# Kernel optimization log

Measured on AMD Instinct MI355X. Metric: run time of the kernel, lower is better.

## Reference

```python
import jax, jax.numpy as jnp
import numpy as np

B, S, D, H, F = 4, 2048, 1024, 16, 4096
HD = D // H
NEG = -2.0 ** 32
EPS = 1e-5


def _gelu(x):
    return x * 0.5 * (1.0 + jax.scipy.special.erf(x / jnp.sqrt(2.0).astype(x.dtype)))


def _layernorm(x, scale, offset):
    mu = jnp.mean(x, axis=-1, keepdims=True)
    var = jnp.mean(jnp.square(x - mu), axis=-1, keepdims=True)
    return (x - mu) * jax.lax.rsqrt(var + EPS) * scale + offset


def setup_inputs() -> dict:
    key = jax.random.key(0)
    ks = jax.random.split(key, 12)
    s = 0.02
    return {
        "x": jax.random.normal(ks[0], (B, S, D), jnp.float32),
        "mask": jnp.zeros((B, S), jnp.int32),  # 1 = masked-out (padding)
        "Wq": jax.random.normal(ks[1], (D, D), jnp.float32) * s,
        "bq": jnp.zeros((D,), jnp.float32),
        "Wk": jax.random.normal(ks[2], (D, D), jnp.float32) * s,
        "bk": jnp.zeros((D,), jnp.float32),
        "Wv": jax.random.normal(ks[3], (D, D), jnp.float32) * s,
        "bv": jnp.zeros((D,), jnp.float32),
        "Wo": jax.random.normal(ks[4], (D, D), jnp.float32) * s,
        "bo": jnp.zeros((D,), jnp.float32),
        "ln1_s": jnp.ones((D,), jnp.float32),
        "ln1_b": jnp.zeros((D,), jnp.float32),
        "W1": jax.random.normal(ks[5], (D, F), jnp.float32) * s,
        "b1": jnp.zeros((F,), jnp.float32),
        "W2": jax.random.normal(ks[6], (F, D), jnp.float32) * s,
        "b2": jnp.zeros((D,), jnp.float32),
        "ln2_s": jnp.ones((D,), jnp.float32),
        "ln2_b": jnp.zeros((D,), jnp.float32),
    }


def reference(x, mask, Wq, bq, Wk, bk, Wv, bv, Wo, bo, ln1_s, ln1_b,
              W1, b1, W2, b2, ln2_s, ln2_b):
    b, s, d = x.shape
    q = (x @ Wq + bq).reshape(b, s, H, HD)
    k = (x @ Wk + bk).reshape(b, s, H, HD)
    v = (x @ Wv + bv).reshape(b, s, H, HD)
    logits = jnp.einsum('btnh,bsnh->bnts', q, k) / jnp.sqrt(jnp.float32(HD))
    logits = logits + (mask.astype(jnp.float32) * NEG)[:, None, None, :]
    attn = jax.nn.softmax(logits, axis=-1)
    ctx = jnp.einsum('bsnh,bnts->btnh', v, attn).reshape(b, s, d)
    attn_out = ctx @ Wo + bo
    h = _layernorm(attn_out + x, ln1_s, ln1_b)
    mlp = _gelu(h @ W1 + b1) @ W2 + b2
    return _layernorm(mlp + h, ln2_s, ln2_b)
```

## Files before the change

kernel.cpp:

```cpp
#include <hip/hip_runtime.h>
#include <hip/hip_bf16.h>

typedef __attribute__((ext_vector_type(8))) short short8;
typedef __attribute__((ext_vector_type(4))) short s16x4;
typedef __attribute__((ext_vector_type(4))) float f32x4;
typedef unsigned short u16;

#define DEV __device__ __forceinline__
#define MFMA32(a, b, c) __builtin_amdgcn_mfma_f32_16x16x32_bf16(a, b, c, 0, 0, 0)
#define MFMA16(a, b, c) __builtin_amdgcn_mfma_f32_16x16x16bf16_1k(a, b, c, 0, 0, 0)

DEV u16 f2b(float f) {
    __hip_bfloat16 h = __float2bfloat16(f);
    return __builtin_bit_cast(unsigned short, h);
}

DEV void gl_lds16(const u16* g, u16* l) {
    __builtin_amdgcn_global_load_lds((const unsigned int*)g, (unsigned int*)l, 16, 0, 0);
}

__global__ __launch_bounds__(256) void cast_bf16(const float* __restrict__ in, u16* __restrict__ out, int n) {
    int i = (blockIdx.x * 256 + threadIdx.x) * 4;
    if (i < n) {
        float4 v = *(const float4*)(in + i);
        ushort4 o;
        o.x = f2b(v.x); o.y = f2b(v.y); o.z = f2b(v.z); o.w = f2b(v.w);
        *(ushort4*)(out + i) = o;
    }
}

__global__ __launch_bounds__(256) void transpose_cast(const float* __restrict__ in, u16* __restrict__ out,
                                                      int R, int C) {
    __shared__ float t[32][33];
    int bx = blockIdx.x * 32;
    int by = blockIdx.y * 32;
    int tx = threadIdx.x, ty = threadIdx.y;
#pragma unroll
    for (int i = 0; i < 32; i += 8) t[ty + i][tx] = in[(size_t)(by + ty + i) * C + bx + tx];
    __syncthreads();
#pragma unroll
    for (int i = 0; i < 32; i += 8) out[(size_t)(bx + ty + i) * R + by + tx] = f2b(t[tx][ty + i]);
}

__global__ __launch_bounds__(256) void pack_bias(const float* __restrict__ bq, const float* __restrict__ bk,
                                                 const float* __restrict__ bv, const float* __restrict__ bo,
                                                 const float* __restrict__ b1, const float* __restrict__ b2,
                                                 float* __restrict__ out) {
    int i = blockIdx.x * 256 + threadIdx.x;
    if (i >= 9216) return;
    float v;
    if (i < 1024) v = bq[i];
    else if (i < 2048) v = bk[i - 1024];
    else if (i < 3072) v = bv[i - 2048];
    else if (i < 4096) v = bo[i - 3072];
    else if (i < 8192) v = b1[i - 4096];
    else v = b2[i - 8192];
    out[i] = v;
}

template <bool GELU, bool BF16OUT>
__global__ __launch_bounds__(256) void gemm_bt(const u16* __restrict__ A, const u16* __restrict__ B,
                                               const float* __restrict__ bias, float* __restrict__ cf,
                                               u16* __restrict__ cb, int M, int N, int K) {
    __shared__ __align__(16) u16 As[128 * 32];
    __shared__ __align__(16) u16 Bs[128 * 32];
    const int tid = threadIdx.x;
    const int wid = tid >> 6, lane = tid & 63;
    const int wr = wid >> 1, wc = wid & 1;
    const int m0 = blockIdx.x * 128, n0 = blockIdx.y * 128;
    const int r16 = lane & 15, g = lane >> 4;
    const int lrow = lane >> 2, lk = (lane & 3) * 8;

    f32x4 acc[4][4];
#pragma unroll
    for (int i = 0; i < 4; i++)
#pragma unroll
        for (int j = 0; j < 4; j++) acc[i][j] = (f32x4){0.f, 0.f, 0.f, 0.f};

    const u16* ga = A + (size_t)(m0 + wid * 32 + lrow) * K + lk;
    const u16* gb = B + (size_t)(n0 + wid * 32 + lrow) * K + lk;
    u16* lA0 = &As[(wid * 32) * 32];
    u16* lA1 = &As[(wid * 32 + 16) * 32];
    u16* lB0 = &Bs[(wid * 32) * 32];
    u16* lB1 = &Bs[(wid * 32 + 16) * 32];

    for (int kt = 0; kt < K; kt += 32) {
        gl_lds16(ga + kt, lA0);
        gl_lds16(ga + (size_t)16 * K + kt, lA1);
        gl_lds16(gb + kt, lB0);
        gl_lds16(gb + (size_t)16 * K + kt, lB1);
        __syncthreads();
        short8 af[4], bfr[4];
#pragma unroll
        for (int i = 0; i < 4; i++) af[i] = *(const short8*)&As[(wr * 64 + i * 16 + r16) * 32 + g * 8];
#pragma unroll
        for (int j = 0; j < 4; j++) bfr[j] = *(const short8*)&Bs[(wc * 64 + j * 16 + r16) * 32 + g * 8];
#pragma unroll
        for (int i = 0; i < 4; i++)
#pragma unroll
            for (int j = 0; j < 4; j++) acc[i][j] = MFMA32(af[i], bfr[j], acc[i][j]);
        __syncthreads();
    }

#pragma unroll
    for (int i = 0; i < 4; i++) {
#pragma unroll
        for (int j = 0; j < 4; j++) {
#pragma unroll
            for (int r = 0; r < 4; r++) {
                int row = m0 + wr * 64 + i * 16 + g * 4 + r;
                int col = n0 + wc * 64 + j * 16 + r16;
                float v = acc[i][j][r] + bias[col];
                if (GELU) v = 0.5f * v * (1.0f + erff(v * 0.70710678118654752f));
                if (BF16OUT) cb[(size_t)row * N + col] = f2b(v);
                else cf[(size_t)row * N + col] = v;
            }
        }
    }
}

__global__ __launch_bounds__(256) void attn_kernel(const u16* __restrict__ qkv, const int* __restrict__ mask,
                                                   u16* __restrict__ ctx) {
    const int tid = threadIdx.x, wid = tid >> 6, lane = tid & 63;
    const int r16 = lane & 15, g = lane >> 4;
    const int h = blockIdx.y, b = blockIdx.z;
    const size_t baserow = (size_t)b * 2048;
    const int q0 = blockIdx.x * 64;

    __shared__ __align__(16) u16 Ks[64 * 64];
    __shared__ __align__(16) u16 Vs[64 * 64];
    __shared__ __align__(16) float mb[64];

    const float SCALE = 0.18033688011112042f;
    const float MNEG = -6.196328018e9f;

    short8 qf0, qf1;
    {
        const u16* qp = qkv + (baserow + q0 + wid * 16 + r16) * 3072 + h * 64 + g * 8;
        qf0 = *(const short8*)qp;
        qf1 = *(const short8*)(qp + 32);
    }

    const int L = lane;
    const int kchunk = (L & 7) ^ (L >> 3);
    const u16* kg0 = qkv + (baserow + wid * 16 + (L >> 3)) * 3072 + 1024 + h * 64 + kchunk * 8;
    const u16* kg1 = kg0 + (size_t)8 * 3072;
    u16* kl0 = &Ks[wid * 1024];
    u16* kl1 = &Ks[wid * 1024 + 512];
    const u16* vg0 = qkv + (baserow + wid * 16 + ((L & 31) >> 1)) * 3072 + 2048 + h * 64
                     + ((L >> 5) * 16 + (L & 1) * 8);
    const u16* vg1 = vg0 + 32;
    u16* vl0 = &Vs[wid * 1024];
    u16* vl1 = &Vs[wid * 1024 + 512];
    const unsigned vaddr = (unsigned)(unsigned long long)&Vs[0] + (unsigned)(r16 * 2 + g * 128);

    f32x4 Ot[4];
#pragma unroll
    for (int dt = 0; dt < 4; dt++) Ot[dt] = (f32x4){0.f, 0.f, 0.f, 0.f};
    float mrun = -1e30f, lrun = 0.f;

    for (int kt = 0; kt < 2048; kt += 64) {
        const size_t go = (size_t)kt * 3072;
        gl_lds16(kg0 + go, kl0);
        gl_lds16(kg1 + go, kl1);
        gl_lds16(vg0 + go, vl0);
        gl_lds16(vg1 + go, vl1);
        if (tid < 64) mb[tid] = mask[baserow + kt + tid] ? MNEG : 0.0f;
        __syncthreads();

        f32x4 z[4];
#pragma unroll
        for (int t = 0; t < 4; t++) {
            const int row = t * 16 + r16;
            const int sw = row & 7;
            short8 a0 = *(const short8*)&Ks[row * 64 + ((g ^ sw) * 8)];
            short8 a1 = *(const short8*)&Ks[row * 64 + (((4 + g) ^ sw) * 8)];
            f32x4 zz = (f32x4){0.f, 0.f, 0.f, 0.f};
            zz = MFMA32(a0, qf0, zz);
            zz = MFMA32(a1, qf1, zz);
            z[t] = zz;
        }

        f32x4 sv[4];
#pragma unroll
        for (int t = 0; t < 4; t++) {
            f32x4 mbv = *(const f32x4*)&mb[t * 16 + g * 4];
            sv[t] = z[t] * SCALE + mbv;
        }

        float pmax = sv[0][0];
#pragma unroll
        for (int t = 0; t < 4; t++)
#pragma unroll
            for (int j = 0; j < 4; j++) pmax = fmaxf(pmax, sv[t][j]);
        pmax = fmaxf(pmax, __shfl_xor(pmax, 16));
        pmax = fmaxf(pmax, __shfl_xor(pmax, 32));

        if (!__all(pmax - mrun <= 11.5f)) {
            float mnew = fmaxf(mrun, pmax);
            float alpha = exp2f(mrun - mnew);
            mrun = mnew;
            lrun *= alpha;
#pragma unroll
            for (int dt = 0; dt < 4; dt++) Ot[dt] *= alpha;
        }

        s16x4 pb[4];
        float rs = 0.f;
#pragma unroll
        for (int t = 0; t < 4; t++) {
            float p0 = exp2f(sv[t][0] - mrun);
            float p1 = exp2f(sv[t][1] - mrun);
            float p2 = exp2f(sv[t][2] - mrun);
            float p3 = exp2f(sv[t][3] - mrun);
            rs += (p0 + p1) + (p2 + p3);
            s16x4 pk;
            pk[0] = (short)f2b(p0); pk[1] = (short)f2b(p1);
            pk[2] = (short)f2b(p2); pk[3] = (short)f2b(p3);
            pb[t] = pk;
        }
        rs += __shfl_xor(rs, 16);
        rs += __shfl_xor(rs, 32);
        lrun += rs;

        s16x4 vf[4][4];
#pragma unroll
        for (int t = 0; t < 4; t++)
#pragma unroll
            for (int dt = 0; dt < 4; dt++)
                asm volatile("ds_read_b64_tr_b16 %0, %1"
                             : "=v"(vf[t][dt])
                             : "v"(vaddr + (unsigned)((t * 4 + dt) * 512)));
        asm volatile("s_waitcnt lgkmcnt(0)" ::: "memory");
        __builtin_amdgcn_sched_barrier(0);
#pragma unroll
        for (int t = 0; t < 4; t++)
#pragma unroll
            for (int dt = 0; dt < 4; dt++) Ot[dt] = MFMA16(vf[t][dt], pb[t], Ot[dt]);
        __syncthreads();
    }

    const float rl = 1.0f / lrun;
    u16* cp = ctx + (baserow + q0 + wid * 16 + r16) * 1024 + h * 64 + g * 4;
#pragma unroll
    for (int dt = 0; dt < 4; dt++) {
        ushort4 o4;
        o4.x = f2b(Ot[dt][0] * rl);
        o4.y = f2b(Ot[dt][1] * rl);
        o4.z = f2b(Ot[dt][2] * rl);
        o4.w = f2b(Ot[dt][3] * rl);
        *(ushort4*)(cp + dt * 16) = o4;
    }
}

__global__ __launch_bounds__(256) void ln_kernel(const float* __restrict__ a, const float* __restrict__ res,
                                                 const float* __restrict__ gamma, const float* __restrict__ beta,
                                                 float* __restrict__ outf, u16* __restrict__ outb) {
    const int row = blockIdx.x, tid = threadIdx.x;
    const size_t base = (size_t)row * 1024 + tid * 4;
    float4 va = *(const float4*)(a + base);
    float4 vr = *(const float4*)(res + base);
    float x0 = va.x + vr.x, x1 = va.y + vr.y, x2 = va.z + vr.z, x3 = va.w + vr.w;
    float s = x0 + x1 + x2 + x3;
    float ss = x0 * x0 + x1 * x1 + x2 * x2 + x3 * x3;
#pragma unroll
    for (int m = 1; m < 64; m <<= 1) { s += __shfl_xor(s, m, 64); ss += __shfl_xor(ss, m, 64); }
    __shared__ float red[8];
    if ((tid & 63) == 0) { red[tid >> 6] = s; red[4 + (tid >> 6)] = ss; }
    __syncthreads();
    s = red[0] + red[1] + red[2] + red[3];
    ss = red[4] + red[5] + red[6] + red[7];
    float mu = s * (1.0f / 1024.0f);
    float var = ss * (1.0f / 1024.0f) - mu * mu;
    float rstd = rsqrtf(var + 1e-5f);
    float4 g4 = *(const float4*)(gamma + tid * 4);
    float4 b4 = *(const float4*)(beta + tid * 4);
    float y0 = (x0 - mu) * rstd * g4.x + b4.x;
    float y1 = (x1 - mu) * rstd * g4.y + b4.y;
    float y2 = (x2 - mu) * rstd * g4.z + b4.z;
    float y3 = (x3 - mu) * rstd * g4.w + b4.w;
    *(float4*)(outf + base) = make_float4(y0, y1, y2, y3);
    if (outb) {
        ushort4 ob;
        ob.x = f2b(y0); ob.y = f2b(y1); ob.z = f2b(y2); ob.w = f2b(y3);
        *(ushort4*)(outb + base) = ob;
    }
}

extern "C" void kernel_launch(void* const* d_in, const int* in_sizes, int n_in, void* d_out, int out_size,
                              void* d_ws, size_t ws_size, hipStream_t stream) {
    const float* x = (const float*)d_in[0];
    const int* mask = (const int*)d_in[1];
    const float* Wq = (const float*)d_in[2];
    const float* bq = (const float*)d_in[3];
    const float* Wk = (const float*)d_in[4];
    const float* bk = (const float*)d_in[5];
    const float* Wv = (const float*)d_in[6];
    const float* bv = (const float*)d_in[7];
    const float* Wo = (const float*)d_in[8];
    const float* bo = (const float*)d_in[9];
    const float* ln1s = (const float*)d_in[10];
    const float* ln1b = (const float*)d_in[11];
    const float* W1 = (const float*)d_in[12];
    const float* b1 = (const float*)d_in[13];
    const float* W2 = (const float*)d_in[14];
    const float* b2 = (const float*)d_in[15];
    const float* ln2s = (const float*)d_in[16];
    const float* ln2b = (const float*)d_in[17];
    float* out = (float*)d_out;
    char* ws = (char*)d_ws;

    const size_t MB = 1024 * 1024;
    u16* XB = (u16*)(ws + 0);
    u16* WTq = (u16*)(ws + 16 * MB);
    u16* WTk = WTq + 1024 * 1024;
    u16* WTv = WTk + 1024 * 1024;
    u16* WTo = WTv + 1024 * 1024;
    u16* WT1 = WTo + 1024 * 1024;
    u16* WT2 = WT1 + 4096 * 1024;
    float* BIAS = (float*)(ws + 40 * MB);
    u16* QKV = (u16*)(ws + 41 * MB);
    u16* CTX = (u16*)(ws + 0);
    float* ATT = (float*)(ws + 41 * MB);
    float* Hbuf = (float*)(ws + 73 * MB);
    u16* HB = (u16*)(ws + 105 * MB);
    u16* MLP1 = (u16*)(ws + 121 * MB);
    float* MLP2 = (float*)(ws + 41 * MB);

    dim3 tb(32, 8);
    cast_bf16<<<8192, 256, 0, stream>>>(x, XB, 8192 * 1024);
    transpose_cast<<<dim3(32, 32), tb, 0, stream>>>(Wq, WTq, 1024, 1024);
    transpose_cast<<<dim3(32, 32), tb, 0, stream>>>(Wk, WTk, 1024, 1024);
    transpose_cast<<<dim3(32, 32), tb, 0, stream>>>(Wv, WTv, 1024, 1024);
    transpose_cast<<<dim3(32, 32), tb, 0, stream>>>(Wo, WTo, 1024, 1024);
    transpose_cast<<<dim3(128, 32), tb, 0, stream>>>(W1, WT1, 1024, 4096);
    transpose_cast<<<dim3(32, 128), tb, 0, stream>>>(W2, WT2, 4096, 1024);
    pack_bias<<<36, 256, 0, stream>>>(bq, bk, bv, bo, b1, b2, BIAS);

    gemm_bt<false, true><<<dim3(64, 24), 256, 0, stream>>>(XB, WTq, BIAS, nullptr, QKV, 8192, 3072, 1024);
    attn_kernel<<<dim3(32, 16, 4), 256, 0, stream>>>(QKV, mask, CTX);
    gemm_bt<false, false><<<dim3(64, 8), 256, 0, stream>>>(CTX, WTo, BIAS + 3072, ATT, nullptr, 8192, 1024, 1024);
    ln_kernel<<<8192, 256, 0, stream>>>(ATT, x, ln1s, ln1b, Hbuf, HB);
    gemm_bt<true, true><<<dim3(64, 32), 256, 0, stream>>>(HB, WT1, BIAS + 4096, nullptr, MLP1, 8192, 4096, 1024);
    gemm_bt<false, false><<<dim3(64, 8), 256, 0, stream>>>(MLP1, WT2, BIAS + 8192, MLP2, nullptr, 8192, 1024, 4096);
    ln_kernel<<<8192, 256, 0, stream>>>(MLP2, Hbuf, ln2s, ln2b, out, nullptr);
}
```

Measured before the change: 554.5 us.

## Replace GEMM with 256-row double-buffered 8-wave kernel and tune attention scheduling

The old 128x128 single-buffered GEMM is replaced by a 512-thread, 8-wave kernel with 256xBN tiles and BK=64. It double-buffers LDS loads with explicit vmcnt waits, XOR-swizzles LDS to avoid bank conflicts, and remaps block IDs so neighbouring blocks reuse the same tiles in cache. The attention kernel raises wave priority around its MFMA sections and uses packed bf16 conversion and tree reductions for max and sum. The GEMM gets more data reuse and overlaps global loads with compute, at the cost of much more LDS per block, which may limit occupancy.

```diff
diff --git a/kernel.cpp b/kernel.cpp
--- a/kernel.cpp
+++ b/kernel.cpp
@@ -9,6 +9,7 @@
 #define DEV __device__ __forceinline__
 #define MFMA32(a, b, c) __builtin_amdgcn_mfma_f32_16x16x32_bf16(a, b, c, 0, 0, 0)
 #define MFMA16(a, b, c) __builtin_amdgcn_mfma_f32_16x16x16bf16_1k(a, b, c, 0, 0, 0)
+#define SBAR() asm volatile("s_barrier" ::: "memory")
 
 DEV u16 f2b(float f) {
     __hip_bfloat16 h = __float2bfloat16(f);
@@ -58,59 +59,100 @@
     out[i] = v;
 }
 
-template <bool GELU, bool BF16OUT>
-__global__ __launch_bounds__(256) void gemm_bt(const u16* __restrict__ A, const u16* __restrict__ B,
-                                               const float* __restrict__ bias, float* __restrict__ cf,
-                                               u16* __restrict__ cb, int M, int N, int K) {
-    __shared__ __align__(16) u16 As[128 * 32];
-    __shared__ __align__(16) u16 Bs[128 * 32];
+template <int BN, bool GELU, bool BF16OUT>
+__global__ __launch_bounds__(512, 2) void gemm8p(const u16* __restrict__ A, const u16* __restrict__ B,
+                                                 const float* __restrict__ bias, float* __restrict__ cf,
+                                                 u16* __restrict__ cb, int M, int N, int K) {
+    constexpr int NREP = BN / 64;
+    constexpr int BLD = BN / 64;
+    __shared__ __align__(16) u16 As[2][256 * 64];
+    __shared__ __align__(16) u16 Bs[2][BN * 64];
+
     const int tid = threadIdx.x;
     const int wid = tid >> 6, lane = tid & 63;
-    const int wr = wid >> 1, wc = wid & 1;
-    const int m0 = blockIdx.x * 128, n0 = blockIdx.y * 128;
+    const int wm = wid >> 2, wn = wid & 3;
     const int r16 = lane & 15, g = lane >> 4;
-    const int lrow = lane >> 2, lk = (lane & 3) * 8;
-
-    f32x4 acc[4][4];
-#pragma unroll
-    for (int i = 0; i < 4; i++)
-#pragma unroll
-        for (int j = 0; j < 4; j++) acc[i][j] = (f32x4){0.f, 0.f, 0.f, 0.f};
-
-    const u16* ga = A + (size_t)(m0 + wid * 32 + lrow) * K + lk;
-    const u16* gb = B + (size_t)(n0 + wid * 32 + lrow) * K + lk;
-    u16* lA0 = &As[(wid * 32) * 32];
-    u16* lA1 = &As[(wid * 32 + 16) * 32];
-    u16* lB0 = &Bs[(wid * 32) * 32];
-    u16* lB1 = &Bs[(wid * 32 + 16) * 32];
-
-    for (int kt = 0; kt < K; kt += 32) {
-        gl_lds16(ga + kt, lA0);
-        gl_lds16(ga + (size_t)16 * K + kt, lA1);
-        gl_lds16(gb + kt, lB0);
-        gl_lds16(gb + (size_t)16 * K + kt, lB1);
-        __syncthreads();
-        short8 af[4], bfr[4];
-#pragma unroll
-        for (int i = 0; i < 4; i++) af[i] = *(const short8*)&As[(wr * 64 + i * 16 + r16) * 32 + g * 8];
-#pragma unroll
-        for (int j = 0; j < 4; j++) bfr[j] = *(const short8*)&Bs[(wc * 64 + j * 16 + r16) * 32 + g * 8];
-#pragma unroll
-        for (int i = 0; i < 4; i++)
-#pragma unroll
-            for (int j = 0; j < 4; j++) acc[i][j] = MFMA32(af[i], bfr[j], acc[i][j]);
-        __syncthreads();
-    }
-
-#pragma unroll
-    for (int i = 0; i < 4; i++) {
-#pragma unroll
-        for (int j = 0; j < 4; j++) {
+
+    const int nwg = gridDim.x;
+    const int mtiles = M >> 8;
+    const int sid = (blockIdx.x & 7) * (nwg >> 3) + (blockIdx.x >> 3);
+    const int bm = sid % mtiles, bn = sid / mtiles;
+
+    const int srow = tid >> 3;
+    const int schunk = (tid & 7) ^ (((tid >> 5) & 1) << 1);
+    const u16* ga = A + (size_t)(bm * 256 + srow) * K + schunk * 8;
+    const u16* gb = B + (size_t)(bn * BN + srow) * K + schunk * 8;
+
+    f32x4 acc[8 * NREP];
+#pragma unroll
+    for (int i = 0; i < 8 * NREP; i++) acc[i] = (f32x4){0.f, 0.f, 0.f, 0.f};
+
+    const int NT = K >> 6;
+#pragma unroll
+    for (int j = 0; j < 4; j++) gl_lds16(ga + (size_t)(j * 64) * K, &As[0][wid * 512 + j * 4096]);
+#pragma unroll
+    for (int j = 0; j < BLD; j++) gl_lds16(gb + (size_t)(j * 64) * K, &Bs[0][wid * 512 + j * 4096]);
+
+    for (int t = 0; t < NT; ++t) {
+        const int c = t & 1, nb = c ^ 1;
+        if (t + 1 < NT) {
+            const int kn = (t + 1) << 6;
+#pragma unroll
+            for (int j = 0; j < 4; j++) gl_lds16(ga + (size_t)(j * 64) * K + kn, &As[nb][wid * 512 + j * 4096]);
+#pragma unroll
+            for (int j = 0; j < BLD; j++) gl_lds16(gb + (size_t)(j * 64) * K + kn, &Bs[nb][wid * 512 + j * 4096]);
+            if constexpr (BN == 256) asm volatile("s_waitcnt vmcnt(8)" ::: "memory");
+            else                     asm volatile("s_waitcnt vmcnt(6)" ::: "memory");
+        } else {
+            asm volatile("s_waitcnt vmcnt(0)" ::: "memory");
+        }
+        SBAR();
+
+        short8 bfr[NREP][2];
+#pragma unroll
+        for (int q = 0; q < 4; q++) {
+            if (q == 0) {
+#pragma unroll
+                for (int n = 0; n < NREP; n++)
+#pragma unroll
+                    for (int ks = 0; ks < 2; ks++) {
+                        int lin = (wn * (BN >> 2) + n * 16 + r16) * 128 + ks * 64 + g * 16;
+                        int off = lin ^ (((lin >> 9) & 1) << 5);
+                        bfr[n][ks] = *(const short8*)((const char*)&Bs[c][0] + off);
+                    }
+            }
+            short8 af[2][2];
+#pragma unroll
+            for (int mm = 0; mm < 2; mm++)
+#pragma unroll
+                for (int ks = 0; ks < 2; ks++) {
+                    int lin = (wm * 128 + (q * 2 + mm) * 16 + r16) * 128 + ks * 64 + g * 16;
+                    int off = lin ^ (((lin >> 9) & 1) << 5);
+                    af[mm][ks] = *(const short8*)((const char*)&As[c][0] + off);
+                }
+            asm volatile("s_waitcnt lgkmcnt(0)" ::: "memory");
+            __builtin_amdgcn_s_setprio(1);
+#pragma unroll
+            for (int mm = 0; mm < 2; mm++)
+#pragma unroll
+                for (int n = 0; n < NREP; n++)
+#pragma unroll
+                    for (int ks = 0; ks < 2; ks++)
+                        acc[(q * 2 + mm) * NREP + n] = MFMA32(af[mm][ks], bfr[n][ks], acc[(q * 2 + mm) * NREP + n]);
+            __builtin_amdgcn_s_setprio(0);
+            SBAR();
+        }
+    }
+
+#pragma unroll
+    for (int m = 0; m < 8; m++) {
+#pragma unroll
+        for (int n = 0; n < NREP; n++) {
 #pragma unroll
             for (int r = 0; r < 4; r++) {
-                int row = m0 + wr * 64 + i * 16 + g * 4 + r;
-                int col = n0 + wc * 64 + j * 16 + r16;
-                float v = acc[i][j][r] + bias[col];
+                int row = bm * 256 + wm * 128 + m * 16 + g * 4 + r;
+                int col = bn * BN + wn * (BN >> 2) + n * 16 + r16;
+                float v = acc[m * NREP + n][r] + bias[col];
                 if (GELU) v = 0.5f * v * (1.0f + erff(v * 0.70710678118654752f));
                 if (BF16OUT) cb[(size_t)row * N + col] = f2b(v);
                 else cf[(size_t)row * N + col] = v;
@@ -169,6 +211,7 @@
         __syncthreads();
 
         f32x4 z[4];
+        __builtin_amdgcn_s_setprio(1);
 #pragma unroll
         for (int t = 0; t < 4; t++) {
             const int row = t * 16 + r16;
@@ -180,6 +223,7 @@
             zz = MFMA32(a1, qf1, zz);
             z[t] = zz;
         }
+        __builtin_amdgcn_s_setprio(0);
 
         f32x4 sv[4];
 #pragma unroll
@@ -188,11 +232,11 @@
             sv[t] = z[t] * SCALE + mbv;
         }
 
-        float pmax = sv[0][0];
-#pragma unroll
-        for (int t = 0; t < 4; t++)
-#pragma unroll
-            for (int j = 0; j < 4; j++) pmax = fmaxf(pmax, sv[t][j]);
+        float mt0 = fmaxf(fmaxf(sv[0][0], sv[0][1]), fmaxf(sv[0][2], sv[0][3]));
+        float mt1 = fmaxf(fmaxf(sv[1][0], sv[1][1]), fmaxf(sv[1][2], sv[1][3]));
+        float mt2 = fmaxf(fmaxf(sv[2][0], sv[2][1]), fmaxf(sv[2][2], sv[2][3]));
+        float mt3 = fmaxf(fmaxf(sv[3][0], sv[3][1]), fmaxf(sv[3][2], sv[3][3]));
+        float pmax = fmaxf(fmaxf(mt0, mt1), fmaxf(mt2, mt3));
         pmax = fmaxf(pmax, __shfl_xor(pmax, 16));
         pmax = fmaxf(pmax, __shfl_xor(pmax, 32));
 
@@ -205,23 +249,28 @@
             for (int dt = 0; dt < 4; dt++) Ot[dt] *= alpha;
         }
 
-        s16x4 pb[4];
-        float rs = 0.f;
+        f32x4 pv[4];
 #pragma unroll
         for (int t = 0; t < 4; t++) {
-            float p0 = exp2f(sv[t][0] - mrun);
-            float p1 = exp2f(sv[t][1] - mrun);
-            float p2 = exp2f(sv[t][2] - mrun);
-            float p3 = exp2f(sv[t][3] - mrun);
-            rs += (p0 + p1) + (p2 + p3);
-            s16x4 pk;
-            pk[0] = (short)f2b(p0); pk[1] = (short)f2b(p1);
-            pk[2] = (short)f2b(p2); pk[3] = (short)f2b(p3);
-            pb[t] = pk;
-        }
+            f32x4 d = sv[t] - mrun;
+            pv[t][0] = exp2f(d[0]); pv[t][1] = exp2f(d[1]);
+            pv[t][2] = exp2f(d[2]); pv[t][3] = exp2f(d[3]);
+        }
+        f32x4 rv = (pv[0] + pv[1]) + (pv[2] + pv[3]);
+        float rs = (rv[0] + rv[1]) + (rv[2] + rv[3]);
         rs += __shfl_xor(rs, 16);
         rs += __shfl_xor(rs, 32);
         lrun += rs;
+
+        s16x4 pb[4];
+#pragma unroll
+        for (int t = 0; t < 4; t++) {
+            unsigned lo, hi;
+            asm("v_cvt_pk_bf16_f32 %0, %1, %2" : "=v"(lo) : "v"(pv[t][0]), "v"(pv[t][1]));
+            asm("v_cvt_pk_bf16_f32 %0, %1, %2" : "=v"(hi) : "v"(pv[t][2]), "v"(pv[t][3]));
+            uint2 u; u.x = lo; u.y = hi;
+            pb[t] = __builtin_bit_cast(s16x4, u);
+        }
 
         s16x4 vf[4][4];
 #pragma unroll
@@ -233,10 +282,12 @@
                              : "v"(vaddr + (unsigned)((t * 4 + dt) * 512)));
         asm volatile("s_waitcnt lgkmcnt(0)" ::: "memory");
         __builtin_amdgcn_sched_barrier(0);
+        __builtin_amdgcn_s_setprio(1);
 #pragma unroll
         for (int t = 0; t < 4; t++)
 #pragma unroll
             for (int dt = 0; dt < 4; dt++) Ot[dt] = MFMA16(vf[t][dt], pb[t], Ot[dt]);
+        __builtin_amdgcn_s_setprio(0);
         __syncthreads();
     }
 
@@ -337,11 +388,11 @@
     transpose_cast<<<dim3(32, 128), tb, 0, stream>>>(W2, WT2, 4096, 1024);
     pack_bias<<<36, 256, 0, stream>>>(bq, bk, bv, bo, b1, b2, BIAS);
 
-    gemm_bt<false, true><<<dim3(64, 24), 256, 0, stream>>>(XB, WTq, BIAS, nullptr, QKV, 8192, 3072, 1024);
+    gemm8p<128, false, true><<<768, 512, 0, stream>>>(XB, WTq, BIAS, nullptr, QKV, 8192, 3072, 1024);
     attn_kernel<<<dim3(32, 16, 4), 256, 0, stream>>>(QKV, mask, CTX);
-    gemm_bt<false, false><<<dim3(64, 8), 256, 0, stream>>>(CTX, WTo, BIAS + 3072, ATT, nullptr, 8192, 1024, 1024);
+    gemm8p<128, false, false><<<256, 512, 0, stream>>>(CTX, WTo, BIAS + 3072, ATT, nullptr, 8192, 1024, 1024);
     ln_kernel<<<8192, 256, 0, stream>>>(ATT, x, ln1s, ln1b, Hbuf, HB);
-    gemm_bt<true, true><<<dim3(64, 32), 256, 0, stream>>>(HB, WT1, BIAS + 4096, nullptr, MLP1, 8192, 4096, 1024);
-    gemm_bt<false, false><<<dim3(64, 8), 256, 0, stream>>>(MLP1, WT2, BIAS + 8192, MLP2, nullptr, 8192, 1024, 4096);
+    gemm8p<256, true, true><<<512, 512, 0, stream>>>(HB, WT1, BIAS + 4096, nullptr, MLP1, 8192, 4096, 1024);
+    gemm8p<128, false, false><<<256, 512, 0, stream>>>(MLP1, WT2, BIAS + 8192, MLP2, nullptr, 8192, 1024, 4096);
     ln_kernel<<<8192, 256, 0, stream>>>(MLP2, Hbuf, ln2s, ln2b, out, nullptr);
 }
```

Result: slower. 586.9 us (+5.8%).

## Compute softmax row sums via MFMA with ones and trim VALU work in attention

Applied to the files above, without the earlier changes.

Drops the per-tile VALU row-sum reduction and its cross-lane shuffles. The softmax denominator is instead accumulated with an extra MFMA that multiplies the bf16 probabilities by a ones fragment, so the sum now uses the rounded bf16 values. The max reduction uses v_max3 and the bf16 packing uses v_cvt_pk_bf16_f32 via inline asm. s_setprio is raised around the MFMA phases. Together these cut VALU pressure in the attention inner loop at the cost of one extra MFMA per key tile.

```diff
diff --git a/kernel.cpp b/kernel.cpp
--- a/kernel.cpp
+++ b/kernel.cpp
@@ -13,6 +13,12 @@
 DEV u16 f2b(float f) {
     __hip_bfloat16 h = __float2bfloat16(f);
     return __builtin_bit_cast(unsigned short, h);
+}
+
+DEV float max3f(float a, float b, float c) {
+    float d;
+    asm("v_max3_f32 %0, %1, %2, %3" : "=v"(d) : "v"(a), "v"(b), "v"(c));
+    return d;
 }
 
 DEV void gl_lds16(const u16* g, u16* l) {
@@ -133,6 +139,7 @@
 
     const float SCALE = 0.18033688011112042f;
     const float MNEG = -6.196328018e9f;
+    const s16x4 ONES = {(short)0x3F80, (short)0x3F80, (short)0x3F80, (short)0x3F80};
 
     short8 qf0, qf1;
     {
@@ -157,7 +164,8 @@
     f32x4 Ot[4];
 #pragma unroll
     for (int dt = 0; dt < 4; dt++) Ot[dt] = (f32x4){0.f, 0.f, 0.f, 0.f};
-    float mrun = -1e30f, lrun = 0.f;
+    f32x4 Osum = (f32x4){0.f, 0.f, 0.f, 0.f};
+    float mrun = -1e30f;
 
     for (int kt = 0; kt < 2048; kt += 64) {
         const size_t go = (size_t)kt * 3072;
@@ -169,17 +177,19 @@
         __syncthreads();
 
         f32x4 z[4];
+        __builtin_amdgcn_s_setprio(1);
 #pragma unroll
         for (int t = 0; t < 4; t++) {
             const int row = t * 16 + r16;
-            const int sw = row & 7;
-            short8 a0 = *(const short8*)&Ks[row * 64 + ((g ^ sw) * 8)];
-            short8 a1 = *(const short8*)&Ks[row * 64 + (((4 + g) ^ sw) * 8)];
+            const int swz = row & 7;
+            short8 a0 = *(const short8*)&Ks[row * 64 + ((g ^ swz) * 8)];
+            short8 a1 = *(const short8*)&Ks[row * 64 + (((4 + g) ^ swz) * 8)];
             f32x4 zz = (f32x4){0.f, 0.f, 0.f, 0.f};
             zz = MFMA32(a0, qf0, zz);
             zz = MFMA32(a1, qf1, zz);
             z[t] = zz;
         }
+        __builtin_amdgcn_s_setprio(0);
 
         f32x4 sv[4];
 #pragma unroll
@@ -188,11 +198,12 @@
             sv[t] = z[t] * SCALE + mbv;
         }
 
-        float pmax = sv[0][0];
-#pragma unroll
-        for (int t = 0; t < 4; t++)
-#pragma unroll
-            for (int j = 0; j < 4; j++) pmax = fmaxf(pmax, sv[t][j]);
+        float m0 = max3f(sv[0][0], sv[0][1], sv[0][2]);
+        float m1 = max3f(sv[0][3], sv[1][0], sv[1][1]);
+        float m2 = max3f(sv[1][2], sv[1][3], sv[2][0]);
+        float m3 = max3f(sv[2][1], sv[2][2], sv[2][3]);
+        float m4 = max3f(sv[3][0], sv[3][1], sv[3][2]);
+        float pmax = fmaxf(max3f(m0, m1, m2), max3f(m3, m4, sv[3][3]));
         pmax = fmaxf(pmax, __shfl_xor(pmax, 16));
         pmax = fmaxf(pmax, __shfl_xor(pmax, 32));
 
@@ -200,28 +211,22 @@
             float mnew = fmaxf(mrun, pmax);
             float alpha = exp2f(mrun - mnew);
             mrun = mnew;
-            lrun *= alpha;
+            Osum *= alpha;
 #pragma unroll
             for (int dt = 0; dt < 4; dt++) Ot[dt] *= alpha;
         }
 
         s16x4 pb[4];
-        float rs = 0.f;
 #pragma unroll
         for (int t = 0; t < 4; t++) {
-            float p0 = exp2f(sv[t][0] - mrun);
-            float p1 = exp2f(sv[t][1] - mrun);
-            float p2 = exp2f(sv[t][2] - mrun);
-            float p3 = exp2f(sv[t][3] - mrun);
-            rs += (p0 + p1) + (p2 + p3);
-            s16x4 pk;
-            pk[0] = (short)f2b(p0); pk[1] = (short)f2b(p1);
-            pk[2] = (short)f2b(p2); pk[3] = (short)f2b(p3);
-            pb[t] = pk;
-        }
-        rs += __shfl_xor(rs, 16);
-        rs += __shfl_xor(rs, 32);
-        lrun += rs;
+            f32x4 d = sv[t] - mrun;
+            float p0 = exp2f(d[0]), p1 = exp2f(d[1]), p2 = exp2f(d[2]), p3 = exp2f(d[3]);
+            unsigned lo, hi;
+            asm("v_cvt_pk_bf16_f32 %0, %1, %2" : "=v"(lo) : "v"(p0), "v"(p1));
+            asm("v_cvt_pk_bf16_f32 %0, %1, %2" : "=v"(hi) : "v"(p2), "v"(p3));
+            uint2 u; u.x = lo; u.y = hi;
+            pb[t] = __builtin_bit_cast(s16x4, u);
+        }
 
         s16x4 vf[4][4];
 #pragma unroll
@@ -233,14 +238,18 @@
                              : "v"(vaddr + (unsigned)((t * 4 + dt) * 512)));
         asm volatile("s_waitcnt lgkmcnt(0)" ::: "memory");
         __builtin_amdgcn_sched_barrier(0);
-#pragma unroll
-        for (int t = 0; t < 4; t++)
+        __builtin_amdgcn_s_setprio(1);
+#pragma unroll
+        for (int t = 0; t < 4; t++) {
 #pragma unroll
             for (int dt = 0; dt < 4; dt++) Ot[dt] = MFMA16(vf[t][dt], pb[t], Ot[dt]);
+            Osum = MFMA16(ONES, pb[t], Osum);
+        }
+        __builtin_amdgcn_s_setprio(0);
         __syncthreads();
     }
 
-    const float rl = 1.0f / lrun;
+    const float rl = 1.0f / Osum[0];
     u16* cp = ctx + (baserow + q0 + wid * 16 + r16) * 1024 + h * 64 + g * 4;
 #pragma unroll
     for (int dt = 0; dt < 4; dt++) {
```

New measurement: 529.0 us. -4.6%, faster.
